# Optimization experiments

Measured on AMD Instinct MI355X. Metric: run time of the kernel, lower is better.

The kernel has to match this reference:

```python
import jax, jax.numpy as jnp
import numpy as np

B, S, D, H, F = 4, 1024, 2048, 16, 8192
HD = D // H  # head dim = 128
EPS = 1e-5


def layer_norm(x, w, b):
    mu = jnp.mean(x, axis=-1, keepdims=True)
    var = jnp.mean(jnp.square(x - mu), axis=-1, keepdims=True)
    return (x - mu) * jax.lax.rsqrt(var + EPS) * w + b


def setup_inputs() -> dict:
    key = jax.random.key(0)
    ks = jax.random.split(key, 12)
    s = 0.02  # realistic init scale for weights
    return {
        "x": jax.random.normal(ks[0], (B, S, D), jnp.float32),
        "attention_mask": jnp.zeros((B, 1, 1, S), jnp.float32),
        "wq": jax.random.normal(ks[1], (D, D), jnp.float32) * s,
        "bq": jax.random.normal(ks[2], (D,), jnp.float32) * s,
        "wk": jax.random.normal(ks[3], (D, D), jnp.float32) * s,
        "bk": jax.random.normal(ks[4], (D,), jnp.float32) * s,
        "wv": jax.random.normal(ks[5], (D, D), jnp.float32) * s,
        "bv": jax.random.normal(ks[6], (D,), jnp.float32) * s,
        "wo": jax.random.normal(ks[7], (D, D), jnp.float32) * s,
        "bo": jax.random.normal(ks[8], (D,), jnp.float32) * s,
        "ln1_w": jnp.ones((D,), jnp.float32),
        "ln1_b": jnp.zeros((D,), jnp.float32),
        "wi": jax.random.normal(ks[9], (F, D), jnp.float32) * s,
        "bi": jax.random.normal(ks[10], (F,), jnp.float32) * s,
        "wo2": jax.random.normal(ks[11], (D, F), jnp.float32) * s,
        "bo2": jnp.zeros((D,), jnp.float32),
        "ln2_w": jnp.ones((D,), jnp.float32),
        "ln2_b": jnp.zeros((D,), jnp.float32),
    }


def reference(x, attention_mask, wq, bq, wk, bk, wv, bv, wo, bo,
              ln1_w, ln1_b, wi, bi, wo2, bo2, ln2_w, ln2_b):
    # --- self attention ---
    q = (jnp.einsum('bsd,ed->bse', x, wq) + bq).reshape(B, S, H, HD).transpose(0, 2, 1, 3)
    k = (jnp.einsum('bsd,ed->bse', x, wk) + bk).reshape(B, S, H, HD).transpose(0, 2, 1, 3)
    v = (jnp.einsum('bsd,ed->bse', x, wv) + bv).reshape(B, S, H, HD).transpose(0, 2, 1, 3)
    scores = jnp.einsum('bhqd,bhkd->bhqk', q, k) / jnp.sqrt(jnp.float32(HD))
    scores = scores + attention_mask  # additive mask, broadcast over heads/query
    probs = jax.nn.softmax(scores, axis=-1)
    ctx = jnp.einsum('bhqk,bhkd->bhqd', probs, v)
    ctx = ctx.transpose(0, 2, 1, 3).reshape(B, S, D)
    # --- attention output: dense + bias + residual + LayerNorm ---
    attn_out = layer_norm(jnp.einsum('bsd,ed->bse', ctx, wo) + bo + x, ln1_w, ln1_b)
    # --- FFN: intermediate dense + bias, GELU, output dense + bias + residual + LN ---
    inter = jnp.einsum('bsd,fd->bsf', attn_out, wi) + bi
    h = jax.nn.gelu(inter, approximate=False)
    out = layer_norm(jnp.einsum('bsf,df->bsd', h, wo2) + bo2 + attn_out, ln2_w, ln2_b)
    return out
```

## Files before the change

### kernel.cpp

```cpp
#include <hip/hip_runtime.h>
#include <hip/hip_bf16.h>
#include <cstdint>
#include <cstddef>

typedef __attribute__((ext_vector_type(8))) short short8;
typedef __attribute__((ext_vector_type(4))) float f32x4;

#define DEV static __device__ __forceinline__

constexpr int kS = 1024, kD = 2048, kH = 16, kHD = 128, kF = 8192;
constexpr int kM = 4096;
constexpr float kEPS = 1e-5f;

constexpr size_t SZ_DD   = (size_t)kD * kD * 2;
constexpr size_t SZ_FD   = (size_t)kF * kD * 2;
constexpr size_t SZ_MD16 = (size_t)kM * kD * 2;
constexpr size_t SZ_MD32 = (size_t)kM * kD * 4;
constexpr size_t OFF_WQ  = 0;
constexpr size_t OFF_WK  = OFF_WQ + SZ_DD;
constexpr size_t OFF_WV  = OFF_WK + SZ_DD;
constexpr size_t OFF_WO  = OFF_WV + SZ_DD;
constexpr size_t OFF_WI  = OFF_WO + SZ_DD;
constexpr size_t OFF_WO2 = OFF_WI + SZ_FD;
constexpr size_t OFF_XB  = OFF_WO2 + SZ_FD;
constexpr size_t OFF_Q   = OFF_XB + SZ_MD16;
constexpr size_t OFF_K   = OFF_Q + SZ_MD16;
constexpr size_t OFF_V   = OFF_K + SZ_MD16;
constexpr size_t OFF_H   = OFF_XB;
constexpr size_t OFF_CTX = OFF_V + SZ_MD16;
constexpr size_t OFF_Y1  = OFF_CTX + SZ_MD16;
constexpr size_t OFF_A1B = OFF_Y1 + SZ_MD32;
constexpr size_t OFF_Y2  = OFF_A1B + SZ_MD16;
constexpr size_t WS_NEED = OFF_Y2 + SZ_MD32;

DEV void gload16(const void* g, void* l) {
  __builtin_amdgcn_global_load_lds(
      (const __attribute__((address_space(1))) unsigned int*)g,
      (__attribute__((address_space(3))) unsigned int*)l, 16, 0, 0);
}

__global__ void cvt_all(const float* __restrict__ x,  const float* __restrict__ wq,
                        const float* __restrict__ wk, const float* __restrict__ wv,
                        const float* __restrict__ wo,
                        const float* __restrict__ bq, const float* __restrict__ bk,
                        const float* __restrict__ bv,
                        __hip_bfloat16* __restrict__ outw, float* __restrict__ bqkv) {
  constexpr int M1 = 1 << 20;
  constexpr int NW = 6 * M1;
  int stride = gridDim.x * blockDim.x;
  for (int i = blockIdx.x * blockDim.x + threadIdx.x; i < NW + 1536; i += stride) {
    if (i < NW) {
      const float* src; int off; int dst;
      if (i < 4 * M1) { src = (i < M1) ? wq : (i < 2 * M1) ? wk : (i < 3 * M1) ? wv : wo;
                        off = i & (M1 - 1); dst = i; }
      else            { src = x; off = i - 4 * M1; dst = i + 8 * M1; }
      float4 v = reinterpret_cast<const float4*>(src)[off];
      union { ushort4 u; __hip_bfloat16 h[4]; } o;
      o.h[0] = __float2bfloat16(v.x);
      o.h[1] = __float2bfloat16(v.y);
      o.h[2] = __float2bfloat16(v.z);
      o.h[3] = __float2bfloat16(v.w);
      reinterpret_cast<ushort4*>(outw)[dst] = o.u;
    } else {
      int j = i - NW;
      const float* src = (j < 512) ? bq : (j < 1024) ? bk : bv;
      reinterpret_cast<float4*>(bqkv)[j] =
          reinterpret_cast<const float4*>(src)[j & 511];
    }
  }
}

template <int MODE>
__global__ __launch_bounds__(512, 2)
void gemm256(const __hip_bfloat16* __restrict__ A,
             const __hip_bfloat16* __restrict__ Bt,
             const float* __restrict__ bias,
             float* __restrict__ out0, float* __restrict__ out1,
             void* __restrict__ outb,
             int M, int N, int K, int kLen) {
  __shared__ __align__(16) char lds[131072];
  const int tid = threadIdx.x;
  const int lane = tid & 63, w = tid >> 6;
  const int wm = w >> 2, wn = w & 3;
  const int hw = w >> 2;
  const int lg = lane >> 4, lr = lane & 15;
  const int gy = M >> 8, gx = N >> 8;
  const int nwg = gridDim.x, orig = blockIdx.x;
  const int l = (orig & 7) * (nwg >> 3) + (orig >> 3);
  const int tilesPer = gx * gy;
  const int spl = l / tilesPer;
  const int rem = l - spl * tilesPer;
  const int bx = rem / gy, by = rem - bx * gy;
  const int m0 = by * 256, n0 = bx * 256;
  const int k0 = spl * kLen;
  const int NT = kLen >> 6;

  const char* gs[8];
  #pragma unroll
  for (int h = 0; h < 4; ++h) {
    const __hip_bfloat16* src = (h < 2) ? A : Bt;
    const int r0 = ((h < 2) ? m0 : n0) + (h & 1) * 128;
    #pragma unroll
    for (int i = 0; i < 2; ++i) {
      int c = i * 512 + tid;
      int row = c >> 3, slot = c & 7;
      gs[h * 2 + i] =
          (const char*)(src + (size_t)(r0 + row) * K + k0 + (slot ^ (row & 7)) * 8);
    }
  }

#define STAGE(P, H, TOFF)                                                          \
  {                                                                                \
    char* dstb = lds + (((H) < 2) ? 0 : 65536) + (P) * 32768 + ((H) & 1) * 16384;  \
    gload16(gs[(H) * 2 + 0] + (TOFF) * 128, dstb + (0 * 512 + tid) * 16);          \
    gload16(gs[(H) * 2 + 1] + (TOFF) * 128, dstb + (1 * 512 + tid) * 16);          \
  }

  auto ldA = [&](int P, int qm, int mr, int kk) {
    int row = qm * 128 + wm * 64 + mr * 16 + lr;
    return *reinterpret_cast<const short8*>(
        lds + P * 32768 + row * 128 + (((kk * 4 + lg) ^ (row & 7)) * 16));
  };
  auto ldB = [&](int P, int qn, int nr, int kk) {
    int row = qn * 128 + wn * 32 + nr * 16 + lr;
    return *reinterpret_cast<const short8*>(
        lds + 65536 + P * 32768 + row * 128 + (((kk * 4 + lg) ^ (row & 7)) * 16));
  };

  f32x4 acc[4][4][2] = {};

#define MFMA_HALF(p, kk, B)                                                     \
  _Pragma("unroll")                                                             \
  for (int mi = 0; mi < 4; ++mi)                                                \
    _Pragma("unroll")                                                           \
    for (int ni = 0; ni < 2; ++ni)                                              \
      acc[p][mi][ni] = __builtin_amdgcn_mfma_f32_16x16x32_bf16(                 \
          av[kk][mi], B[kk][ni], acc[p][mi][ni], 0, 0, 0);

#define WAIT_LGKM(n)                                                            \
  asm volatile("s_waitcnt lgkmcnt(" #n ")" ::: "memory");                       \
  __builtin_amdgcn_sched_barrier(0);

#define TILE_BODY(P, PF)                                                        \
  {                                                                             \
    asm volatile("s_waitcnt vmcnt(0)" ::: "memory");                            \
    __builtin_amdgcn_s_barrier();                                               \
    _Pragma("unroll")                                                           \
    for (int i = 0; i < 4; ++i) av[0][i] = ldA(P, hw, i, 0);                    \
    _Pragma("unroll")                                                           \
    for (int i = 0; i < 2; ++i) b0[0][i] = ldB(P, hw, i, 0);                    \
    _Pragma("unroll")                                                           \
    for (int i = 0; i < 4; ++i) av[1][i] = ldA(P, hw, i, 1);                    \
    _Pragma("unroll")                                                           \
    for (int i = 0; i < 2; ++i) b0[1][i] = ldB(P, hw, i, 1);                    \
    if (PF) { STAGE((P) ^ 1, 0, 1 + (P)) STAGE((P) ^ 1, 2, 1 + (P)) }           \
    WAIT_LGKM(6)                                                                \
    __builtin_amdgcn_s_setprio(1);                                              \
    MFMA_HALF(0, 0, b0)                                                         \
    WAIT_LGKM(0)                                                                \
    MFMA_HALF(0, 1, b0)                                                         \
    __builtin_amdgcn_s_setprio(0);                                              \
    _Pragma("unroll")                                                           \
    for (int i = 0; i < 2; ++i) b1[0][i] = ldB(P, 1 - hw, i, 0);                \
    _Pragma("unroll")                                                           \
    for (int i = 0; i < 2; ++i) b1[1][i] = ldB(P, 1 - hw, i, 1);                \
    if (PF) { STAGE((P) ^ 1, 3, 1 + (P)) STAGE((P) ^ 1, 1, 1 + (P)) }           \
    WAIT_LGKM(2)                                                                \
    __builtin_amdgcn_s_setprio(1);                                              \
    MFMA_HALF(1, 0, b1)                                                         \
    WAIT_LGKM(0)                                                                \
    MFMA_HALF(1, 1, b1)                                                         \
    __builtin_amdgcn_s_setprio(0);                                              \
    _Pragma("unroll")                                                           \
    for (int i = 0; i < 4; ++i) av[0][i] = ldA(P, 1 - hw, i, 0);                \
    _Pragma("unroll")                                                           \
    for (int i = 0; i < 4; ++i) av[1][i] = ldA(P, 1 - hw, i, 1);                \
    WAIT_LGKM(4)                                                                \
    __builtin_amdgcn_s_setprio(1);                                              \
    MFMA_HALF(2, 0, b1)                                                         \
    WAIT_LGKM(0)                                                                \
    MFMA_HALF(2, 1, b1)                                                         \
    __builtin_amdgcn_s_setprio(0);                                              \
    _Pragma("unroll")                                                           \
    for (int i = 0; i < 2; ++i) b0[0][i] = ldB(P, hw, i, 0);                    \
    _Pragma("unroll")                                                           \
    for (int i = 0; i < 2; ++i) b0[1][i] = ldB(P, hw, i, 1);                    \
    WAIT_LGKM(2)                                                                \
    __builtin_amdgcn_s_setprio(1);                                              \
    MFMA_HALF(3, 0, b0)                                                         \
    WAIT_LGKM(0)                                                                \
    MFMA_HALF(3, 1, b0)                                                         \
    __builtin_amdgcn_s_setprio(0);                                              \
  }

  STAGE(0, 0, 0) STAGE(0, 2, 0) STAGE(0, 3, 0) STAGE(0, 1, 0)

  for (int t2 = 0; t2 < NT; t2 += 2) {
    short8 av[2][4], b0[2][2], b1[2][2];
    TILE_BODY(0, true)
    TILE_BODY(1, (t2 + 2 < NT))
    #pragma unroll
    for (int j = 0; j < 8; ++j) gs[j] += 256;
  }
#undef TILE_BODY
#undef MFMA_HALF
#undef WAIT_LGKM
#undef STAGE

  #pragma unroll
  for (int p = 0; p < 4; ++p) {
    const int qm = (p < 2) ? hw : 1 - hw;
    const int qn = (p == 0 || p == 3) ? hw : 1 - hw;
    #pragma unroll
    for (int ni = 0; ni < 2; ++ni) {
      int col = n0 + qn * 128 + wn * 32 + ni * 16 + lr;
      float bvv = 0.f;
      if constexpr (MODE != 3) bvv = bias[col];
      #pragma unroll
      for (int mi = 0; mi < 4; ++mi) {
        int row0 = m0 + qm * 128 + wm * 64 + mi * 16 + lg * 4;
        #pragma unroll
        for (int r = 0; r < 4; ++r) {
          int row = row0 + r;
          float val = acc[p][mi][ni][r] + bvv;
          if constexpr (MODE == 0) {
            int which = col >> 11;
            int d = col & 2047;
            int hh = d >> 7, hd = d & 127;
            int bb = row >> 10, ss = row & 1023;
            __hip_bfloat16* base = (__hip_bfloat16*)outb + (size_t)which * ((size_t)kM * kD);
            base[(((size_t)(bb * kH + hh)) * kS + ss) * kHD + hd] = __float2bfloat16(val);
          } else if constexpr (MODE == 2) {
            float g = 0.5f * val * (1.0f + erff(val * 0.70710678118654752f));
            ((__hip_bfloat16*)outb)[(size_t)row * N + col] = __float2bfloat16(g);
          } else {
            float* o = spl ? out1 : out0;
            o[(size_t)row * N + col] = val;
          }
        }
      }
    }
  }
}

__global__ __launch_bounds__(512, 2)
void attn_fwd(const __hip_bfloat16* __restrict__ q,
              const __hip_bfloat16* __restrict__ k,
              const __hip_bfloat16* __restrict__ v,
              const float* __restrict__ mask,
              __hip_bfloat16* __restrict__ ctx,
              const float* __restrict__ wi, const float* __restrict__ wo2,
              __hip_bfloat16* __restrict__ outw ) {
  __shared__ __align__(16) char Ks[2][64 * 256];
  __shared__ __align__(16) char Vt[2][128 * 128];
  __shared__ __align__(16) char Ps[8][2048];
  const int tid = threadIdx.x, lane = tid & 63, w = tid >> 6;
  const int lg = lane >> 4, lr = lane & 15;
  const int orig = blockIdx.x;
  const int l = (orig & 7) * 32 + (orig >> 3);
  const int qp = l & 3, bh = l >> 2;
  const int b = bh >> 4;
  const int s4 = tid >> 5, hd4 = tid & 31;

  short8 qf[2][4];
  #pragma unroll
  for (int s = 0; s < 2; ++s) {
    const __hip_bfloat16* qp_ =
        q + ((size_t)bh * kS + qp * 256 + s * 128 + w * 16 + lr) * kHD + lg * 8;
    #pragma unroll
    for (int kk = 0; kk < 4; ++kk)
      qf[s][kk] = *reinterpret_cast<const short8*>(qp_ + kk * 32);
  }

  auto stageK = [&](int bufi, int t) {
    #pragma unroll
    for (int i = 0; i < 2; ++i) {
      int c = i * 512 + tid;
      int row = c >> 4, slot = c & 15;
      gload16(k + ((size_t)bh * kS + t * 64 + row) * kHD + (slot ^ (row & 15)) * 8,
              Ks[bufi] + c * 16);
    }
  };
  union VU { uint2 u; ushort s[4]; };
  VU vr[4];
  auto loadV = [&](int t) {
    #pragma unroll
    for (int i = 0; i < 4; ++i)
      vr[i].u = *reinterpret_cast<const uint2*>(
          v + ((size_t)bh * kS + t * 64 + s4 * 4 + i) * kHD + hd4 * 4);
  };
  auto writeV = [&](int bufi) {
    #pragma unroll
    for (int j = 0; j < 4; ++j) {
      int hd = hd4 * 4 + j;
      ushort4 o4;
      o4.x = vr[0].s[j]; o4.y = vr[1].s[j]; o4.z = vr[2].s[j]; o4.w = vr[3].s[j];
      *reinterpret_cast<ushort4*>(
          Vt[bufi] + hd * 128 + (((s4 >> 1) ^ (hd & 7)) << 4) + ((s4 & 1) << 3)) = o4;
    }
  };
  float4 cw[4];
  auto cvLoad = [&](int t) {
    int g0 = ((orig * 16 + t) * 512 + tid) * 4;
    #pragma unroll
    for (int j = 0; j < 4; ++j) {
      int g = g0 + j;
      const float* src = (g < (4 << 20)) ? wi : wo2;
      int off = g & ((4 << 20) - 1);
      cw[j] = reinterpret_cast<const float4*>(src)[off];
    }
  };
  auto cvStore = [&](int t) {
    int g0 = ((orig * 16 + t) * 512 + tid) * 4;
    #pragma unroll
    for (int j = 0; j < 4; ++j) {
      union { ushort4 u; __hip_bfloat16 h[4]; } o4;
      o4.h[0] = __float2bfloat16(cw[j].x);
      o4.h[1] = __float2bfloat16(cw[j].y);
      o4.h[2] = __float2bfloat16(cw[j].z);
      o4.h[3] = __float2bfloat16(cw[j].w);
      reinterpret_cast<ushort4*>(outw)[(4 << 20) + g0 + j] = o4.u;
    }
  };

  f32x4 o[2][8] = {};
  float mrun[2][4], lrun[2][4];
  #pragma unroll
  for (int s = 0; s < 2; ++s)
    #pragma unroll
    for (int r = 0; r < 4; ++r) { mrun[s][r] = -1e30f; lrun[s][r] = 0.f; }
  const float scale = 0.08838834764831845f;

  stageK(0, 0);
  loadV(0);
  writeV(0);
  __syncthreads();

  int buf = 0;
  for (int t = 0; t < 16; ++t) {
    if (t + 1 < 16) { stageK(buf ^ 1, t + 1); loadV(t + 1); }
    cvLoad(t);

    float mv[4];
    #pragma unroll
    for (int j = 0; j < 4; ++j) mv[j] = mask[(size_t)b * kS + t * 64 + j * 16 + lr];

    #pragma unroll
    for (int s = 0; s < 2; ++s) {
      f32x4 sacc[4] = {};
      #pragma unroll
      for (int j = 0; j < 4; ++j) {
        int key = j * 16 + lr;
        #pragma unroll
        for (int kk = 0; kk < 4; ++kk) {
          short8 bfrag = *reinterpret_cast<const short8*>(
              Ks[buf] + key * 256 + (((kk * 4 + lg) ^ (key & 15)) * 16));
          sacc[j] = __builtin_amdgcn_mfma_f32_16x16x32_bf16(qf[s][kk], bfrag, sacc[j], 0, 0, 0);
        }
      }
      float sarr[4][4];
      #pragma unroll
      for (int j = 0; j < 4; ++j)
        #pragma unroll
        for (int r = 0; r < 4; ++r) sarr[j][r] = sacc[j][r] * scale + mv[j];
      #pragma unroll
      for (int r = 0; r < 4; ++r) {
        float tm = fmaxf(fmaxf(sarr[0][r], sarr[1][r]), fmaxf(sarr[2][r], sarr[3][r]));
        #pragma unroll
        for (int d = 1; d < 16; d <<= 1) tm = fmaxf(tm, __shfl_xor(tm, d));
        float mnew = fmaxf(mrun[s][r], tm);
        float alpha = __expf(mrun[s][r] - mnew);
        mrun[s][r] = mnew;
        float rs = 0.f;
        #pragma unroll
        for (int j = 0; j < 4; ++j) {
          float p = __expf(sarr[j][r] - mnew);
          sarr[j][r] = p;
          rs += p;
        }
        #pragma unroll
        for (int d = 1; d < 16; d <<= 1) rs += __shfl_xor(rs, d);
        lrun[s][r] = lrun[s][r] * alpha + rs;
        #pragma unroll
        for (int n = 0; n < 8; ++n) o[s][n][r] *= alpha;
      }
      #pragma unroll
      for (int r = 0; r < 4; ++r) {
        int qr = lg * 4 + r;
        #pragma unroll
        for (int j = 0; j < 4; ++j)
          *reinterpret_cast<__hip_bfloat16*>(
              Ps[w] + ((qr * 128 + (j * 16 + lr) * 2) ^ ((qr & 7) << 4))) =
              __float2bfloat16(sarr[j][r]);
      }
      #pragma unroll
      for (int kk2 = 0; kk2 < 2; ++kk2) {
        short8 pa = *reinterpret_cast<const short8*>(
            Ps[w] + ((lr * 128 + kk2 * 64 + lg * 16) ^ ((lr & 7) << 4)));
        #pragma unroll
        for (int n = 0; n < 8; ++n) {
          int hd = n * 16 + lr;
          short8 vb = *reinterpret_cast<const short8*>(
              Vt[buf] + hd * 128 + (((kk2 * 4 + lg) ^ (hd & 7)) * 16));
          o[s][n] = __builtin_amdgcn_mfma_f32_16x16x32_bf16(pa, vb, o[s][n], 0, 0, 0);
        }
      }
    }
    cvStore(t);
    if (t + 1 < 16) writeV(buf ^ 1);
    __syncthreads();
    buf ^= 1;
  }

  const int h = bh & 15;
  #pragma unroll
  for (int s = 0; s < 2; ++s)
    #pragma unroll
    for (int r = 0; r < 4; ++r) {
      float inv = 1.0f / lrun[s][r];
      int srow = qp * 256 + s * 128 + w * 16 + lg * 4 + r;
      __hip_bfloat16* cp = ctx + ((size_t)b * kS + srow) * kD + h * 128 + lr;
      #pragma unroll
      for (int n = 0; n < 8; ++n) cp[n * 16] = __float2bfloat16(o[s][n][r] * inv);
    }
}

template <bool WB16>
__global__ void ln_fuse(const float* __restrict__ p0, const float* __restrict__ p1,
                        const float* __restrict__ bias, const float* __restrict__ res,
                        const float* __restrict__ w, const float* __restrict__ b,
                        float* __restrict__ outf, __hip_bfloat16* __restrict__ outb) {
  const int row = blockIdx.x, tid = threadIdx.x;
  const size_t base = (size_t)row * kD;
  float v[8];
  #pragma unroll
  for (int i = 0; i < 2; ++i) {
    int c4 = tid * 2 + i;
    float4 a  = reinterpret_cast<const float4*>(p0 + base)[c4];
    float4 bb = reinterpret_cast<const float4*>(p1 + base)[c4];
    float4 rr = reinterpret_cast<const float4*>(res + base)[c4];
    float4 bs = reinterpret_cast<const float4*>(bias)[c4];
    v[i * 4 + 0] = a.x + bb.x + rr.x + bs.x;
    v[i * 4 + 1] = a.y + bb.y + rr.y + bs.y;
    v[i * 4 + 2] = a.z + bb.z + rr.z + bs.z;
    v[i * 4 + 3] = a.w + bb.w + rr.w + bs.w;
  }
  float s = 0.f;
  #pragma unroll
  for (int i = 0; i < 8; ++i) s += v[i];
  #pragma unroll
  for (int off = 32; off > 0; off >>= 1) s += __shfl_down(s, off);
  __shared__ float r1[4], r2[4];
  if ((tid & 63) == 0) r1[tid >> 6] = s;
  __syncthreads();
  float mean = (r1[0] + r1[1] + r1[2] + r1[3]) * (1.0f / kD);
  float qv = 0.f;
  #pragma unroll
  for (int i = 0; i < 8; ++i) { float d = v[i] - mean; qv += d * d; }
  #pragma unroll
  for (int off = 32; off > 0; off >>= 1) qv += __shfl_down(qv, off);
  if ((tid & 63) == 0) r2[tid >> 6] = qv;
  __syncthreads();
  float rstd = rsqrtf((r2[0] + r2[1] + r2[2] + r2[3]) * (1.0f / kD) + kEPS);
  #pragma unroll
  for (int i = 0; i < 8; ++i) {
    int col = tid * 8 + i;
    float ov = (v[i] - mean) * rstd * w[col] + b[col];
    outf[base + col] = ov;
    if constexpr (WB16) outb[base + col] = __float2bfloat16(ov);
  }
}

extern "C" void kernel_launch(void* const* d_in, const int* in_sizes, int n_in,
                              void* d_out, int out_size, void* d_ws, size_t ws_size,
                              hipStream_t stream) {
  (void)in_sizes; (void)n_in; (void)out_size;
  if (ws_size < WS_NEED) return;
  const float* x    = (const float*)d_in[0];
  const float* mask = (const float*)d_in[1];
  const float* wq   = (const float*)d_in[2];
  const float* bq   = (const float*)d_in[3];
  const float* wk   = (const float*)d_in[4];
  const float* bk   = (const float*)d_in[5];
  const float* wv   = (const float*)d_in[6];
  const float* bv   = (const float*)d_in[7];
  const float* wo   = (const float*)d_in[8];
  const float* bo   = (const float*)d_in[9];
  const float* l1w  = (const float*)d_in[10];
  const float* l1b  = (const float*)d_in[11];
  const float* wi   = (const float*)d_in[12];
  const float* bi   = (const float*)d_in[13];
  const float* wo2  = (const float*)d_in[14];
  const float* bo2  = (const float*)d_in[15];
  const float* l2w  = (const float*)d_in[16];
  const float* l2b  = (const float*)d_in[17];

  char* ws = (char*)d_ws;
  __hip_bfloat16* wqb  = (__hip_bfloat16*)(ws + OFF_WQ);
  __hip_bfloat16* wob  = (__hip_bfloat16*)(ws + OFF_WO);
  __hip_bfloat16* wib  = (__hip_bfloat16*)(ws + OFF_WI);
  __hip_bfloat16* wo2b = (__hip_bfloat16*)(ws + OFF_WO2);
  __hip_bfloat16* xb   = (__hip_bfloat16*)(ws + OFF_XB);
  __hip_bfloat16* qb   = (__hip_bfloat16*)(ws + OFF_Q);
  __hip_bfloat16* kb2  = (__hip_bfloat16*)(ws + OFF_K);
  __hip_bfloat16* vb2  = (__hip_bfloat16*)(ws + OFF_V);
  __hip_bfloat16* hb   = (__hip_bfloat16*)(ws + OFF_H);
  __hip_bfloat16* ctxb = (__hip_bfloat16*)(ws + OFF_CTX);
  __hip_bfloat16* a1b  = (__hip_bfloat16*)(ws + OFF_A1B);
  float* y1   = (float*)(ws + OFF_Y1);
  float* y2   = (float*)(ws + OFF_Y2);
  float* f2p  = (float*)(ws + OFF_WQ);
  float* bqkv = (float*)(ws + OFF_Y2);

  cvt_all<<<2048, 256, 0, stream>>>(x, wq, wk, wv, wo, bq, bk, bv, wqb, bqkv);

  dim3 blk(512);
  gemm256<0><<<dim3(384), blk, 0, stream>>>(
      xb, wqb, bqkv, nullptr, nullptr, qb, kM, 6144, kD, kD);
  attn_fwd<<<dim3(256), dim3(512), 0, stream>>>(qb, kb2, vb2, mask, ctxb, wi, wo2, wqb);
  gemm256<3><<<dim3(256), blk, 0, stream>>>(
      ctxb, wob, nullptr, y1, y2, nullptr, kM, kD, kD, kD / 2);
  ln_fuse<true><<<kM, 256, 0, stream>>>(y1, y2, bo, x, l1w, l1b, y1, a1b);
  gemm256<2><<<dim3(512), blk, 0, stream>>>(
      a1b, wib, bi, nullptr, nullptr, hb, kM, kF, kD, kD);
  gemm256<3><<<dim3(256), blk, 0, stream>>>(
      hb, wo2b, nullptr, y2, f2p, nullptr, kM, kD, kF, kF / 2);
  ln_fuse<false><<<kM, 256, 0, stream>>>(y2, f2p, bo2, y1, l2w, l2b, (float*)d_out, nullptr);
}
```

Baseline: 594.6 us.

## Store QKV row-major and fold Wo conversion into attention kernel

The QKV projection now writes a plain row-major [M, 6144] bf16 buffer instead of scattering into per-head Q/K/V layouts, and the attention kernel reads Q, K and V with a 6144-element row stride. The fp32-to-bf16 conversion of Wo moves out of the up-front conversion kernel and into the attention kernel's spare load/store slots, next to the existing Wi/Wo2 conversion. The goal is cheaper, more coalesced GEMM epilogue stores and a shorter serial conversion phase. The cost is strided K/V/Q reads in attention and some extra global traffic inside the attention loop.

Measured after the change: 587.5 us. No clear change (-1.2%).

```diff
diff --git a/kernel.cpp b/kernel.cpp
--- a/kernel.cpp
+++ b/kernel.cpp
@@ -10,6 +10,7 @@
 
 constexpr int kS = 1024, kD = 2048, kH = 16, kHD = 128, kF = 8192;
 constexpr int kM = 4096;
+constexpr int kDQKV = 6144;
 constexpr float kEPS = 1e-5f;
 
 constexpr size_t SZ_DD   = (size_t)kD * kD * 2;
@@ -24,10 +25,8 @@
 constexpr size_t OFF_WO2 = OFF_WI + SZ_FD;
 constexpr size_t OFF_XB  = OFF_WO2 + SZ_FD;
 constexpr size_t OFF_Q   = OFF_XB + SZ_MD16;
-constexpr size_t OFF_K   = OFF_Q + SZ_MD16;
-constexpr size_t OFF_V   = OFF_K + SZ_MD16;
 constexpr size_t OFF_H   = OFF_XB;
-constexpr size_t OFF_CTX = OFF_V + SZ_MD16;
+constexpr size_t OFF_CTX = OFF_Q + 3 * SZ_MD16;
 constexpr size_t OFF_Y1  = OFF_CTX + SZ_MD16;
 constexpr size_t OFF_A1B = OFF_Y1 + SZ_MD32;
 constexpr size_t OFF_Y2  = OFF_A1B + SZ_MD16;
@@ -41,19 +40,18 @@
 
 __global__ void cvt_all(const float* __restrict__ x,  const float* __restrict__ wq,
                         const float* __restrict__ wk, const float* __restrict__ wv,
-                        const float* __restrict__ wo,
                         const float* __restrict__ bq, const float* __restrict__ bk,
                         const float* __restrict__ bv,
                         __hip_bfloat16* __restrict__ outw, float* __restrict__ bqkv) {
   constexpr int M1 = 1 << 20;
-  constexpr int NW = 6 * M1;
+  constexpr int NW = 5 * M1;
   int stride = gridDim.x * blockDim.x;
   for (int i = blockIdx.x * blockDim.x + threadIdx.x; i < NW + 1536; i += stride) {
     if (i < NW) {
       const float* src; int off; int dst;
-      if (i < 4 * M1) { src = (i < M1) ? wq : (i < 2 * M1) ? wk : (i < 3 * M1) ? wv : wo;
+      if (i < 3 * M1) { src = (i < M1) ? wq : (i < 2 * M1) ? wk : wv;
                         off = i & (M1 - 1); dst = i; }
-      else            { src = x; off = i - 4 * M1; dst = i + 8 * M1; }
+      else            { src = x; off = i - 3 * M1; dst = i + 9 * M1; }
       float4 v = reinterpret_cast<const float4*>(src)[off];
       union { ushort4 u; __hip_bfloat16 h[4]; } o;
       o.h[0] = __float2bfloat16(v.x);
@@ -224,12 +222,7 @@
           int row = row0 + r;
           float val = acc[p][mi][ni][r] + bvv;
           if constexpr (MODE == 0) {
-            int which = col >> 11;
-            int d = col & 2047;
-            int hh = d >> 7, hd = d & 127;
-            int bb = row >> 10, ss = row & 1023;
-            __hip_bfloat16* base = (__hip_bfloat16*)outb + (size_t)which * ((size_t)kM * kD);
-            base[(((size_t)(bb * kH + hh)) * kS + ss) * kHD + hd] = __float2bfloat16(val);
+            ((__hip_bfloat16*)outb)[(size_t)row * N + col] = __float2bfloat16(val);
           } else if constexpr (MODE == 2) {
             float g = 0.5f * val * (1.0f + erff(val * 0.70710678118654752f));
             ((__hip_bfloat16*)outb)[(size_t)row * N + col] = __float2bfloat16(g);
@@ -244,11 +237,10 @@
 }
 
 __global__ __launch_bounds__(512, 2)
-void attn_fwd(const __hip_bfloat16* __restrict__ q,
-              const __hip_bfloat16* __restrict__ k,
-              const __hip_bfloat16* __restrict__ v,
+void attn_fwd(const __hip_bfloat16* __restrict__ qkv,
               const float* __restrict__ mask,
               __hip_bfloat16* __restrict__ ctx,
+              const float* __restrict__ wo,
               const float* __restrict__ wi, const float* __restrict__ wo2,
               __hip_bfloat16* __restrict__ outw ) {
   __shared__ __align__(16) char Ks[2][64 * 256];
@@ -259,14 +251,16 @@
   const int orig = blockIdx.x;
   const int l = (orig & 7) * 32 + (orig >> 3);
   const int qp = l & 3, bh = l >> 2;
-  const int b = bh >> 4;
+  const int b = bh >> 4, h = bh & 15;
   const int s4 = tid >> 5, hd4 = tid & 31;
+  const size_t rb = (size_t)b * kS;
+  const int hc = h * kHD;
 
   short8 qf[2][4];
   #pragma unroll
   for (int s = 0; s < 2; ++s) {
     const __hip_bfloat16* qp_ =
-        q + ((size_t)bh * kS + qp * 256 + s * 128 + w * 16 + lr) * kHD + lg * 8;
+        qkv + (rb + qp * 256 + s * 128 + w * 16 + lr) * kDQKV + hc + lg * 8;
     #pragma unroll
     for (int kk = 0; kk < 4; ++kk)
       qf[s][kk] = *reinterpret_cast<const short8*>(qp_ + kk * 32);
@@ -277,7 +271,7 @@
     for (int i = 0; i < 2; ++i) {
       int c = i * 512 + tid;
       int row = c >> 4, slot = c & 15;
-      gload16(k + ((size_t)bh * kS + t * 64 + row) * kHD + (slot ^ (row & 15)) * 8,
+      gload16(qkv + (rb + t * 64 + row) * kDQKV + kD + hc + (slot ^ (row & 15)) * 8,
               Ks[bufi] + c * 16);
     }
   };
@@ -287,7 +281,7 @@
     #pragma unroll
     for (int i = 0; i < 4; ++i)
       vr[i].u = *reinterpret_cast<const uint2*>(
-          v + ((size_t)bh * kS + t * 64 + s4 * 4 + i) * kHD + hd4 * 4);
+          qkv + (rb + t * 64 + s4 * 4 + i) * kDQKV + 2 * kD + hc + hd4 * 4);
   };
   auto writeV = [&](int bufi) {
     #pragma unroll
@@ -299,7 +293,7 @@
           Vt[bufi] + hd * 128 + (((s4 >> 1) ^ (hd & 7)) << 4) + ((s4 & 1) << 3)) = o4;
     }
   };
-  float4 cw[4];
+  float4 cw[4]; float4 cwo;
   auto cvLoad = [&](int t) {
     int g0 = ((orig * 16 + t) * 512 + tid) * 4;
     #pragma unroll
@@ -309,17 +303,28 @@
       int off = g & ((4 << 20) - 1);
       cw[j] = reinterpret_cast<const float4*>(src)[off];
     }
+    int slot = (orig * 16 + t) * 512 + tid;
+    if (slot < (1 << 20)) cwo = reinterpret_cast<const float4*>(wo)[slot];
   };
   auto cvStore = [&](int t) {
     int g0 = ((orig * 16 + t) * 512 + tid) * 4;
     #pragma unroll
     for (int j = 0; j < 4; ++j) {
-      union { ushort4 u; __hip_bfloat16 h[4]; } o4;
-      o4.h[0] = __float2bfloat16(cw[j].x);
-      o4.h[1] = __float2bfloat16(cw[j].y);
-      o4.h[2] = __float2bfloat16(cw[j].z);
-      o4.h[3] = __float2bfloat16(cw[j].w);
+      union { ushort4 u; __hip_bfloat16 hh[4]; } o4;
+      o4.hh[0] = __float2bfloat16(cw[j].x);
+      o4.hh[1] = __float2bfloat16(cw[j].y);
+      o4.hh[2] = __float2bfloat16(cw[j].z);
+      o4.hh[3] = __float2bfloat16(cw[j].w);
       reinterpret_cast<ushort4*>(outw)[(4 << 20) + g0 + j] = o4.u;
+    }
+    int slot = (orig * 16 + t) * 512 + tid;
+    if (slot < (1 << 20)) {
+      union { ushort4 u; __hip_bfloat16 hh[4]; } o4;
+      o4.hh[0] = __float2bfloat16(cwo.x);
+      o4.hh[1] = __float2bfloat16(cwo.y);
+      o4.hh[2] = __float2bfloat16(cwo.z);
+      o4.hh[3] = __float2bfloat16(cwo.w);
+      reinterpret_cast<ushort4*>(outw)[(3 << 20) + slot] = o4.u;
     }
   };
 
@@ -412,14 +417,13 @@
     buf ^= 1;
   }
 
-  const int h = bh & 15;
   #pragma unroll
   for (int s = 0; s < 2; ++s)
     #pragma unroll
     for (int r = 0; r < 4; ++r) {
       float inv = 1.0f / lrun[s][r];
       int srow = qp * 256 + s * 128 + w * 16 + lg * 4 + r;
-      __hip_bfloat16* cp = ctx + ((size_t)b * kS + srow) * kD + h * 128 + lr;
+      __hip_bfloat16* cp = ctx + (rb + srow) * kD + hc + lr;
       #pragma unroll
       for (int n = 0; n < 8; ++n) cp[n * 16] = __float2bfloat16(o[s][n][r] * inv);
     }
@@ -501,9 +505,7 @@
   __hip_bfloat16* wib  = (__hip_bfloat16*)(ws + OFF_WI);
   __hip_bfloat16* wo2b = (__hip_bfloat16*)(ws + OFF_WO2);
   __hip_bfloat16* xb   = (__hip_bfloat16*)(ws + OFF_XB);
-  __hip_bfloat16* qb   = (__hip_bfloat16*)(ws + OFF_Q);
-  __hip_bfloat16* kb2  = (__hip_bfloat16*)(ws + OFF_K);
-  __hip_bfloat16* vb2  = (__hip_bfloat16*)(ws + OFF_V);
+  __hip_bfloat16* qkvb = (__hip_bfloat16*)(ws + OFF_Q);
   __hip_bfloat16* hb   = (__hip_bfloat16*)(ws + OFF_H);
   __hip_bfloat16* ctxb = (__hip_bfloat16*)(ws + OFF_CTX);
   __hip_bfloat16* a1b  = (__hip_bfloat16*)(ws + OFF_A1B);
@@ -512,12 +514,12 @@
   float* f2p  = (float*)(ws + OFF_WQ);
   float* bqkv = (float*)(ws + OFF_Y2);
 
-  cvt_all<<<2048, 256, 0, stream>>>(x, wq, wk, wv, wo, bq, bk, bv, wqb, bqkv);
+  cvt_all<<<2048, 256, 0, stream>>>(x, wq, wk, wv, bq, bk, bv, wqb, bqkv);
 
   dim3 blk(512);
   gemm256<0><<<dim3(384), blk, 0, stream>>>(
-      xb, wqb, bqkv, nullptr, nullptr, qb, kM, 6144, kD, kD);
-  attn_fwd<<<dim3(256), dim3(512), 0, stream>>>(qb, kb2, vb2, mask, ctxb, wi, wo2, wqb);
+      xb, wqb, bqkv, nullptr, nullptr, qkvb, kM, kDQKV, kD, kD);
+  attn_fwd<<<dim3(256), dim3(512), 0, stream>>>(qkvb, mask, ctxb, wo, wi, wo2, wqb);
   gemm256<3><<<dim3(256), blk, 0, stream>>>(
       ctxb, wob, nullptr, y1, y2, nullptr, kM, kD, kD, kD / 2);
   ln_fuse<true><<<kM, 256, 0, stream>>>(y1, y2, bo, x, l1w, l1b, y1, a1b);
```
